# Performance work log

Measured on AMD Instinct MI355X. Metric: run time of the kernel, lower is better.

## Reference

```python
import jax, jax.numpy as jnp
import numpy as np

B, L, H, T, C = 64, 1024, 512, 100, 97


def setup_inputs() -> dict:
    key = jax.random.key(0)
    k1, k2, k3, k4, k5 = jax.random.split(key, 5)
    return {
        "position_fmap": jax.random.normal(k1, (B, L, H), dtype=jnp.float32),
        "origin_fmap": jax.random.normal(k2, (B, L, H), dtype=jnp.float32),
        "pos_emb": jax.random.normal(k3, (T, H), dtype=jnp.float32),
        "W_gen": jax.random.normal(k4, (C, H), dtype=jnp.float32) * (1.0 / np.sqrt(H)),
        "b_gen": jax.random.normal(k5, (C,), dtype=jnp.float32) * 0.01,
    }


def reference(position_fmap, origin_fmap, pos_emb, W_gen, b_gen):
    # The torch loop over t in [0, T) computes, per step, scores = fmap @ emb_t,
    # softmax over L, then context = a^T @ origin_fmap. Batched over all steps:
    scores = jnp.einsum('blh,th->btl', position_fmap, pos_emb)   # [B, T, L]
    attn = jax.nn.softmax(scores, axis=-1)                       # softmax over spatial L
    context = jnp.einsum('btl,blh->bth', attn, origin_fmap)      # [B, T, H]
    # generator: Linear(H -> num_classes)
    return jnp.einsum('bth,ch->btc', context, W_gen) + b_gen     # [B, T, C]
```

## Files before the change

### kernel.cpp

```cpp
#include <hip/hip_runtime.h>

#define B_   64
#define L_   1024
#define H_   512
#define T_   100
#define C_   97
#define TP_  112

typedef _Float16 h8 __attribute__((ext_vector_type(8)));
typedef __attribute__((ext_vector_type(4))) float f32x4;

__global__ __launch_bounds__(256) void k0_prep(
    const float* __restrict__ emb, const float* __restrict__ W,
    _Float16* __restrict__ e2, _Float16* __restrict__ w2) {
  const int row = blockIdx.x, tid = threadIdx.x;
  if (row < TP_) {
    for (int j = tid; j < H_; j += 256) {
      float v = (row < T_) ? emb[(size_t)row * H_ + j] : 0.f;
      e2[((size_t)(j >> 3) * TP_ + row) * 8 + (j & 7)] = (_Float16)v;
    }
  } else {
    const int c = row - TP_;
    for (int j = tid; j < H_; j += 256) {
      float v = (c < C_) ? W[(size_t)c * H_ + j] : 0.f;
      w2[((size_t)(j >> 3) * TP_ + c) * 8 + (j & 7)] = (_Float16)v;
    }
  }
}

__global__ __launch_bounds__(256, 4) void k12_fused(
    const float* __restrict__ fmap, const float* __restrict__ origin,
    const _Float16* __restrict__ e2, const _Float16* __restrict__ w2,
    _Float16* __restrict__ scT, _Float16* __restrict__ GT,
    float* __restrict__ part) {
  __shared__ float red_m[4][TP_];
  __shared__ float red_s[4][TP_];
  __shared__ float sMb[TP_];
  const int tid = threadIdx.x;
  const int wave = tid >> 6, lane = tid & 63;
  const int quad = lane >> 4, cc = lane & 15;
  const int b = blockIdx.x >> 4;
  const int lb = (blockIdx.x & 15) * 64 + wave * 16 + cc;

  f32x4 accS[7], accG[7];
#pragma unroll
  for (int i = 0; i < 7; ++i) {
    accS[i] = (f32x4){0.f, 0.f, 0.f, 0.f};
    accG[i] = (f32x4){0.f, 0.f, 0.f, 0.f};
  }

  const float* fp = fmap   + ((size_t)b * L_ + lb) * H_ + quad * 8;
  const float* op = origin + ((size_t)b * L_ + lb) * H_ + quad * 8;
  const _Float16* ep = e2 + (size_t)(quad * TP_ + cc) * 8;
  const _Float16* wp = w2 + (size_t)(quad * TP_ + cc) * 8;

#pragma unroll 2
  for (int k = 0; k < H_; k += 32) {
    float4 x0 = *(const float4*)(fp + k);
    float4 x1 = *(const float4*)(fp + k + 4);
    float4 y0 = *(const float4*)(op + k);
    float4 y1 = *(const float4*)(op + k + 4);
    const _Float16* ek = ep + (size_t)(k >> 3) * (TP_ * 8);
    const _Float16* wk = wp + (size_t)(k >> 3) * (TP_ * 8);
    h8 bf, bo;
    bf[0] = (_Float16)x0.x; bf[1] = (_Float16)x0.y;
    bf[2] = (_Float16)x0.z; bf[3] = (_Float16)x0.w;
    bf[4] = (_Float16)x1.x; bf[5] = (_Float16)x1.y;
    bf[6] = (_Float16)x1.z; bf[7] = (_Float16)x1.w;
    bo[0] = (_Float16)y0.x; bo[1] = (_Float16)y0.y;
    bo[2] = (_Float16)y0.z; bo[3] = (_Float16)y0.w;
    bo[4] = (_Float16)y1.x; bo[5] = (_Float16)y1.y;
    bo[6] = (_Float16)y1.z; bo[7] = (_Float16)y1.w;
#pragma unroll
    for (int i = 0; i < 7; ++i) {
      h8 ae = *(const h8*)(ek + i * 128);
      accS[i] = __builtin_amdgcn_mfma_f32_16x16x32_f16(ae, bf, accS[i], 0, 0, 0);
      h8 aw = *(const h8*)(wk + i * 128);
      accG[i] = __builtin_amdgcn_mfma_f32_16x16x32_f16(aw, bo, accG[i], 0, 0, 0);
    }
  }

#pragma unroll
  for (int i = 0; i < 7; ++i) {
#pragma unroll
    for (int r = 0; r < 4; ++r) {
      float m = accS[i][r];
#pragma unroll
      for (int d = 1; d < 16; d <<= 1) m = fmaxf(m, __shfl_xor(m, d, 64));
      float e = __expf(accS[i][r] - m);
#pragma unroll
      for (int d = 1; d < 16; d <<= 1) e += __shfl_xor(e, d, 64);
      if (cc == 0) {
        red_m[wave][i * 16 + quad * 4 + r] = m;
        red_s[wave][i * 16 + quad * 4 + r] = e;
      }
    }
  }
  __syncthreads();
  if (tid < TP_) {
    float M = red_m[0][tid], S = red_s[0][tid];
#pragma unroll
    for (int w = 1; w < 4; ++w) {
      float om = red_m[w][tid], os = red_s[w][tid];
      float nM = fmaxf(M, om);
      S = S * __expf(M - nM) + os * __expf(om - nM);
      M = nM;
    }
    float* p = part + ((size_t)blockIdx.x * TP_ + tid) * 2;
    p[0] = M; p[1] = S;
    sMb[tid] = M;
  }
  __syncthreads();

  _Float16* sp = scT + (size_t)b * TP_ * L_ + lb;
  _Float16* gp = GT  + (size_t)b * TP_ * L_ + lb;
#pragma unroll
  for (int i = 0; i < 7; ++i) {
#pragma unroll
    for (int r = 0; r < 4; ++r) {
      const int t = i * 16 + quad * 4 + r;
      sp[(size_t)t * L_] = (_Float16)(accS[i][r] - sMb[t]);
      gp[(size_t)t * L_] = (_Float16)accG[i][r];
    }
  }
}

__global__ __launch_bounds__(512) void k3_out(
    const _Float16* __restrict__ scT, const _Float16* __restrict__ GT,
    const float* __restrict__ part, const float* __restrict__ bias,
    float* __restrict__ out) {
  __shared__ float sAdj[16][16];
  __shared__ float sInv[16];
  __shared__ f32x4 sred[8][4][64];
  const int bid = blockIdx.x;
  const int b = bid / 14;
  const int rem = bid % 14;
  const int mt = rem >> 1;
  const int ng = rem & 1;
  const int NT = ng ? 3 : 4;
  const int ncol0 = ng * 64;
  const int tid = threadIdx.x;
  const int w = tid >> 6, lane = tid & 63;
  const int quad = lane >> 4, cc = lane & 15;

  if (tid < 16) {
    const int t = mt * 16 + tid;
    float mM[16];
    float M = -1e30f, S = 0.f;
#pragma unroll
    for (int s = 0; s < 16; ++s) {
      const float* p = part + ((size_t)(b * 16 + s) * TP_ + t) * 2;
      float om = p[0], os = p[1];
      mM[s] = om;
      float nM = fmaxf(M, om);
      S = S * __expf(M - nM) + os * __expf(om - nM);
      M = nM;
    }
    sInv[tid] = 1.f / S;
#pragma unroll
    for (int s = 0; s < 16; ++s) sAdj[s][tid] = mM[s] - M;
  }
  __syncthreads();

  f32x4 acc[4];
#pragma unroll
  for (int i = 0; i < 4; ++i) acc[i] = (f32x4){0.f, 0.f, 0.f, 0.f};

  const float inv = sInv[cc];
  const _Float16* ap = scT + ((size_t)(b * TP_ + mt * 16 + cc)) * L_ + quad * 8;
  const _Float16* gp = GT  + ((size_t)(b * TP_ + ncol0 + cc)) * L_ + quad * 8;
  const int kbase = w * 128;
#pragma unroll
  for (int l0 = kbase; l0 < kbase + 128; l0 += 32) {
    const float adj = sAdj[(l0 + quad * 8) >> 6][cc];
    h8 v = *(const h8*)(ap + l0);
    h8 a;
#pragma unroll
    for (int j = 0; j < 8; ++j)
      a[j] = (_Float16)(__expf((float)v[j] + adj) * inv);
#pragma unroll
    for (int nt = 0; nt < 4; ++nt) {
      if (nt < NT) {
        h8 bf = *(const h8*)(gp + (size_t)(nt * 16) * L_ + l0);
        acc[nt] = __builtin_amdgcn_mfma_f32_16x16x32_f16(a, bf, acc[nt], 0, 0, 0);
      }
    }
  }

#pragma unroll
  for (int nt = 0; nt < 4; ++nt)
    if (nt < NT) sred[w][nt][lane] = acc[nt];
  __syncthreads();

  if (w < NT) {
    f32x4 s = sred[0][w][lane];
#pragma unroll
    for (int ww = 1; ww < 8; ++ww) s += sred[ww][w][lane];
    const int c = ncol0 + w * 16 + cc;
    if (c < C_) {
      const float bv = bias[c];
#pragma unroll
      for (int r = 0; r < 4; ++r) {
        const int t = mt * 16 + quad * 4 + r;
        if (t < T_) out[((size_t)b * T_ + t) * C_ + c] = s[r] + bv;
      }
    }
  }
}

extern "C" void kernel_launch(void* const* d_in, const int* in_sizes, int n_in,
                              void* d_out, int out_size, void* d_ws, size_t ws_size,
                              hipStream_t stream) {
  const float* fmap   = (const float*)d_in[0];
  const float* origin = (const float*)d_in[1];
  const float* emb    = (const float*)d_in[2];
  const float* W      = (const float*)d_in[3];
  const float* bias   = (const float*)d_in[4];
  float* out = (float*)d_out;

  char* ws = (char*)d_ws;
  _Float16* e2   = (_Float16*)(ws);
  _Float16* w2   = (_Float16*)(ws + 114688);
  _Float16* scT  = (_Float16*)(ws + 229376);
  float*    part = (float*)   (ws + 14909440);
  _Float16* GT   = (_Float16*)(ws + 15826944);

  hipLaunchKernelGGL(k0_prep,   dim3(224),  dim3(256), 0, stream, emb, W, e2, w2);
  hipLaunchKernelGGL(k12_fused, dim3(1024), dim3(256), 0, stream,
                     fmap, origin, e2, w2, scT, GT, part);
  hipLaunchKernelGGL(k3_out,    dim3(896),  dim3(512), 0, stream,
                     scT, GT, part, bias, out);
}
```

Baseline: 357.7 us.

## Double-buffer fmap/origin tiles in LDS via async global_load_lds

Rewrites the main K loop of the fused score/G kernel so that fp32 fmap and origin rows are staged into a double-buffered LDS tile with global_load_lds, prefetching the next 32-column slice while MFMAs run on the current one. The per-thread strided global float4 loads become coalesced row loads, and the e2/w2 fragments are hoisted ahead of the MFMA chain. The cost is extra LDS (about 32KB), a block barrier every iteration, and launch bounds lowered from 4 to 3 blocks per SM, which reduces occupancy.

```diff
diff --git a/kernel.cpp b/kernel.cpp
--- a/kernel.cpp
+++ b/kernel.cpp
@@ -28,11 +28,19 @@
   }
 }
 
-__global__ __launch_bounds__(256, 4) void k12_fused(
+__device__ __forceinline__ void gl_lds16(const float* g, float* l) {
+  __builtin_amdgcn_global_load_lds(
+      (const __attribute__((address_space(1))) unsigned int*)g,
+      (__attribute__((address_space(3))) unsigned int*)l, 16, 0, 0);
+}
+
+__global__ __launch_bounds__(256, 3) void k12_fused(
     const float* __restrict__ fmap, const float* __restrict__ origin,
     const _Float16* __restrict__ e2, const _Float16* __restrict__ w2,
     _Float16* __restrict__ scT, _Float16* __restrict__ GT,
     float* __restrict__ part) {
+  __shared__ float sF[2][8][64][4];
+  __shared__ float sO[2][8][64][4];
   __shared__ float red_m[4][TP_];
   __shared__ float red_s[4][TP_];
   __shared__ float sMb[TP_];
@@ -40,7 +48,8 @@
   const int wave = tid >> 6, lane = tid & 63;
   const int quad = lane >> 4, cc = lane & 15;
   const int b = blockIdx.x >> 4;
-  const int lb = (blockIdx.x & 15) * 64 + wave * 16 + cc;
+  const int lb0 = (blockIdx.x & 15) * 64;
+  const int rr = wave * 16 + cc;
 
   f32x4 accS[7], accG[7];
 #pragma unroll
@@ -49,19 +58,43 @@
     accG[i] = (f32x4){0.f, 0.f, 0.f, 0.f};
   }
 
-  const float* fp = fmap   + ((size_t)b * L_ + lb) * H_ + quad * 8;
-  const float* op = origin + ((size_t)b * L_ + lb) * H_ + quad * 8;
+  const size_t srow = (size_t)(b * L_ + lb0 + lane) * H_;
+  const int u0 = wave * 2, u1 = wave * 2 + 1;
   const _Float16* ep = e2 + (size_t)(quad * TP_ + cc) * 8;
   const _Float16* wp = w2 + (size_t)(quad * TP_ + cc) * 8;
 
-#pragma unroll 2
-  for (int k = 0; k < H_; k += 32) {
-    float4 x0 = *(const float4*)(fp + k);
-    float4 x1 = *(const float4*)(fp + k + 4);
-    float4 y0 = *(const float4*)(op + k);
-    float4 y1 = *(const float4*)(op + k + 4);
+  gl_lds16(fmap   + srow + 0 + u0 * 4, &sF[0][u0][0][0]);
+  gl_lds16(fmap   + srow + 0 + u1 * 4, &sF[0][u1][0][0]);
+  gl_lds16(origin + srow + 0 + u0 * 4, &sO[0][u0][0][0]);
+  gl_lds16(origin + srow + 0 + u1 * 4, &sO[0][u1][0][0]);
+  __syncthreads();
+
+#pragma unroll 1
+  for (int it = 0; it < 16; ++it) {
+    const int k = it * 32;
+    const int cur = it & 1;
+
     const _Float16* ek = ep + (size_t)(k >> 3) * (TP_ * 8);
     const _Float16* wk = wp + (size_t)(k >> 3) * (TP_ * 8);
+    h8 ae[7], aw[7];
+#pragma unroll
+    for (int i = 0; i < 7; ++i) ae[i] = *(const h8*)(ek + i * 128);
+#pragma unroll
+    for (int i = 0; i < 7; ++i) aw[i] = *(const h8*)(wk + i * 128);
+
+    if (it < 15) {
+      const int kn = k + 32;
+      const int nb = cur ^ 1;
+      gl_lds16(fmap   + srow + kn + u0 * 4, &sF[nb][u0][0][0]);
+      gl_lds16(fmap   + srow + kn + u1 * 4, &sF[nb][u1][0][0]);
+      gl_lds16(origin + srow + kn + u0 * 4, &sO[nb][u0][0][0]);
+      gl_lds16(origin + srow + kn + u1 * 4, &sO[nb][u1][0][0]);
+    }
+
+    float4 x0 = *(const float4*)&sF[cur][2 * quad][rr][0];
+    float4 x1 = *(const float4*)&sF[cur][2 * quad + 1][rr][0];
+    float4 y0 = *(const float4*)&sO[cur][2 * quad][rr][0];
+    float4 y1 = *(const float4*)&sO[cur][2 * quad + 1][rr][0];
     h8 bf, bo;
     bf[0] = (_Float16)x0.x; bf[1] = (_Float16)x0.y;
     bf[2] = (_Float16)x0.z; bf[3] = (_Float16)x0.w;
@@ -71,13 +104,15 @@
     bo[2] = (_Float16)y0.z; bo[3] = (_Float16)y0.w;
     bo[4] = (_Float16)y1.x; bo[5] = (_Float16)y1.y;
     bo[6] = (_Float16)y1.z; bo[7] = (_Float16)y1.w;
-#pragma unroll
-    for (int i = 0; i < 7; ++i) {
-      h8 ae = *(const h8*)(ek + i * 128);
-      accS[i] = __builtin_amdgcn_mfma_f32_16x16x32_f16(ae, bf, accS[i], 0, 0, 0);
-      h8 aw = *(const h8*)(wk + i * 128);
-      accG[i] = __builtin_amdgcn_mfma_f32_16x16x32_f16(aw, bo, accG[i], 0, 0, 0);
-    }
+
+#pragma unroll
+    for (int i = 0; i < 7; ++i)
+      accS[i] = __builtin_amdgcn_mfma_f32_16x16x32_f16(ae[i], bf, accS[i], 0, 0, 0);
+#pragma unroll
+    for (int i = 0; i < 7; ++i)
+      accG[i] = __builtin_amdgcn_mfma_f32_16x16x32_f16(aw[i], bo, accG[i], 0, 0, 0);
+
+    __syncthreads();
   }
 
 #pragma unroll
@@ -112,6 +147,7 @@
   }
   __syncthreads();
 
+  const int lb = lb0 + rr;
   _Float16* sp = scT + (size_t)b * TP_ * L_ + lb;
   _Float16* gp = GT  + (size_t)b * TP_ * L_ + lb;
 #pragma unroll
```

Result: faster. 336.3 us (-6.0%).
